# Kernel tuning notes

Hardware: AMD Instinct MI355X
Metric: run time of the kernel (lower is better)

Reference implementation:

```python
import jax, jax.numpy as jnp
import numpy as np
import math


def _alibi_slopes(n_heads):
    def pow2_slopes(n):
        start = 2.0 ** (-2.0 ** (-(math.log2(n) - 3)))
        return [start * start ** i for i in range(n)]
    if math.log2(n_heads) % 1 == 0:
        return np.array(pow2_slopes(n_heads), dtype=np.float32)
    closest = 2 ** math.floor(math.log2(n_heads))
    base = pow2_slopes(closest)
    extra = pow2_slopes(2 * closest)[0::2][: n_heads - closest]
    return np.array(base + extra, dtype=np.float32)


def setup_inputs() -> dict:
    key = jax.random.key(0)
    ks = jax.random.split(key, 5)
    B, T, D = 2, 2048, 1024
    scale = 1.0 / math.sqrt(D)
    return {
        "x": jax.random.normal(ks[0], (B, T, D), dtype=jnp.float32),
        "Wq": jax.random.normal(ks[1], (D, D), dtype=jnp.float32) * scale,
        "Wk": jax.random.normal(ks[2], (D, D), dtype=jnp.float32) * scale,
        "Wv": jax.random.normal(ks[3], (D, D), dtype=jnp.float32) * scale,
        "Wo": jax.random.normal(ks[4], (D, D), dtype=jnp.float32) * scale,
        "window": 256,
    }


def reference(x, Wq, Wk, Wv, Wo, window):
    B, T, D = x.shape
    H = 16
    d_k = D // H

    def proj(W):
        # torch nn.Linear: y = x @ W.T ; then (B,T,H,dk) -> (B,H,T,dk)
        return (x @ W.T).reshape(B, T, H, d_k).transpose(0, 2, 1, 3)

    Q, K, V = proj(Wq), proj(Wk), proj(Wv)
    scores = jnp.einsum("bhtk,bhsk->bhts", Q, K) / math.sqrt(d_k)

    pos = jnp.arange(T)
    dist = jnp.abs(pos[None, :] - pos[:, None]).astype(jnp.float32)  # (T,T)
    slopes = jnp.asarray(_alibi_slopes(H))  # (H,)
    alibi = -slopes[:, None, None] * dist  # (H,T,T)
    win_mask = jnp.where(dist > window // 2, -jnp.inf, 0.0)  # (T,T)

    scores = scores + alibi[None] + win_mask[None, None]
    attn = jax.nn.softmax(scores, axis=-1)  # dropout=0.0 (eval)
    out = jnp.einsum("bhts,bhsd->bthd", attn, V).reshape(B, T, D)
    return out @ Wo.T, attn
```

## Files before the change

### kernel.cpp

```cpp
#include <hip/hip_runtime.h>
#include <hip/hip_bf16.h>


typedef __bf16 bf16x8 __attribute__((ext_vector_type(8)));
typedef float f32x4 __attribute__((ext_vector_type(4)));

__device__ __forceinline__ float bf2f(unsigned short u) {
    union { unsigned int i; float f; } v; v.i = ((unsigned int)u) << 16; return v.f;
}
__device__ __forceinline__ unsigned short f2bf(float f) {
    union { float f; unsigned int i; } v; v.f = f;
    unsigned int r = v.i + 0x7FFFu + ((v.i >> 16) & 1u);
    return (unsigned short)(r >> 16);
}

__global__ __launch_bounds__(256) void cast_all(
    const float* __restrict__ x,
    const float* __restrict__ wq, const float* __restrict__ wk,
    const float* __restrict__ wv, const float* __restrict__ wo,
    unsigned short* __restrict__ xb, unsigned short* __restrict__ wb)
{
    const int slice = blockIdx.y;
    const int i = (blockIdx.x * 256 + threadIdx.x) * 4;
    const float* src;
    unsigned short* dst;
    if (slice < 4) {
        src = x + (size_t)slice * 1048576;
        dst = xb + (size_t)slice * 1048576;
    } else {
        const float* ws4[4] = {wq, wk, wv, wo};
        src = ws4[slice - 4];
        dst = wb + (size_t)(slice - 4) * 1048576;
    }
    const float4 v = *(const float4*)(src + i);
    ushort4 o;
    o.x = f2bf(v.x); o.y = f2bf(v.y); o.z = f2bf(v.z); o.w = f2bf(v.w);
    *(ushort4*)(dst + i) = o;
}

#define GLDS16(g, l) __builtin_amdgcn_global_load_lds(                      \
    (const __attribute__((address_space(1))) void*)(g),                     \
    (__attribute__((address_space(3))) void*)(l), 16, 0, 0)

__global__ __launch_bounds__(256) void gemm_bf16_nt(
    const unsigned short* __restrict__ A, const unsigned short* __restrict__ Bm,
    float* __restrict__ C, unsigned short* __restrict__ qkv,
    int M, int N, int K, int mode)
{
    __shared__ __align__(16) unsigned short As[128 * 32];
    __shared__ __align__(16) unsigned short Bs[128 * 32];

    const int tid  = threadIdx.x;
    const int lane = tid & 63, w = tid >> 6;
    const int bm = blockIdx.y * 128, bn = blockIdx.x * 128;

    const unsigned short* ga = A  + (size_t)(bm + w * 16 + (lane >> 2)) * K + (lane & 3) * 8;
    const unsigned short* gb = Bm + (size_t)(bn + w * 16 + (lane >> 2)) * K + (lane & 3) * 8;
    unsigned short* laA0 = &As[w * 512];
    unsigned short* laA1 = &As[2048 + w * 512];
    unsigned short* laB0 = &Bs[w * 512];
    unsigned short* laB1 = &Bs[2048 + w * 512];

    const int wr = w >> 1, wc = w & 1;
    const int fr = lane & 15, fq = lane >> 4;

    f32x4 acc[4][4] = {};

    for (int k0 = 0; k0 < K; k0 += 32) {
        GLDS16(ga + k0, laA0);
        GLDS16(ga + k0 + (size_t)64 * K, laA1);
        GLDS16(gb + k0, laB0);
        GLDS16(gb + k0 + (size_t)64 * K, laB1);
        __syncthreads();
        bf16x8 af[4], bfv[4];
#pragma unroll
        for (int i = 0; i < 4; ++i)
            af[i] = *(const bf16x8*)&As[(wr * 64 + i * 16 + fr) * 32 + fq * 8];
#pragma unroll
        for (int j = 0; j < 4; ++j)
            bfv[j] = *(const bf16x8*)&Bs[(wc * 64 + j * 16 + fr) * 32 + fq * 8];
#pragma unroll
        for (int i = 0; i < 4; ++i)
#pragma unroll
            for (int j = 0; j < 4; ++j)
                acc[i][j] = __builtin_amdgcn_mfma_f32_16x16x32_bf16(af[i], bfv[j], acc[i][j], 0, 0, 0);
        __syncthreads();
    }

#pragma unroll
    for (int i = 0; i < 4; ++i) {
#pragma unroll
        for (int j = 0; j < 4; ++j) {
            const int mb = bm + wr * 64 + i * 16 + fq * 4;
            const int n  = bn + wc * 64 + j * 16 + fr;
#pragma unroll
            for (int r = 0; r < 4; ++r) {
                const int m = mb + r;
                const float val = acc[i][j][r];
                if (mode == 0) {
                    C[(size_t)m * N + n] = val;
                } else {
                    const int which = n >> 10, hh = (n >> 6) & 15, dd = n & 63;
                    const int bb = m >> 11, tt = m & 2047;
                    size_t off;
                    if (which == 2)
                        off = (size_t)2 * 4194304 + (((size_t)bb * 16 + hh) * 64 + dd) * 2048 + tt;
                    else
                        off = (size_t)which * 4194304 + (((size_t)bb * 16 + hh) * 2048 + tt) * 64 + dd;
                    qkv[off] = f2bf(val);
                }
            }
        }
    }
}

#define NT_MAX 20
__global__ __launch_bounds__(256) void attn_mfma(
    const unsigned short* __restrict__ Q, const unsigned short* __restrict__ K,
    const unsigned short* __restrict__ VT, float* __restrict__ attn,
    unsigned short* __restrict__ ao, const int* __restrict__ wptr)
{
    const int T = 2048;
    __shared__ __align__(16) unsigned short Plds[4][16][328];

    const int bid = (int)blockIdx.x;
    const int swz = (bid & 7) * 128 + (bid >> 3);
    const int w = threadIdx.x >> 6, lane = threadIdx.x & 63;
    const int fr = lane & 15, fq = lane >> 4;

    const int tblk = swz & 31;
    const int h    = (swz >> 5) & 15;
    const int b    = swz >> 9;
    const int t0   = tblk * 64;

    const int W2 = wptr[0] >> 1;
    const int sA = (t0 - W2) > 0 ? (t0 - W2) : 0;
    int sB = t0 + 63 + W2; if (sB > T - 1) sB = T - 1;
    const int sEnd = sB + 1;
    const int nt  = (sEnd - sA) >> 4;
    const int ncc = (nt + 1) >> 1;

    const size_t bhT = ((size_t)b * 16 + h) * T;
    const unsigned short* Qbh  = Q  + bhT * 64;
    const unsigned short* Kbh  = K  + bhT * 64;
    const unsigned short* VTbh = VT + (((size_t)b * 16 + h) * 64) * T;

    bf16x8 aq0 = *(const bf16x8*)(Qbh + (size_t)(t0 + w * 16 + fr) * 64 + fq * 8);
    bf16x8 aq1 = *(const bf16x8*)(Qbh + (size_t)(t0 + w * 16 + fr) * 64 + 32 + fq * 8);

    const float slope = exp2f(-0.5f * (float)(h + 1));
    const int trow0 = t0 + w * 16 + fq * 4;

    f32x4 sc[NT_MAX];
#pragma unroll
    for (int st = 0; st < NT_MAX; ++st) {
        const int sbase = sA + st * 16;
        if (sbase < sEnd) {
            const unsigned short* kb = Kbh + (size_t)(sbase + fr) * 64 + fq * 8;
            bf16x8 b0 = *(const bf16x8*)(kb);
            bf16x8 b1 = *(const bf16x8*)(kb + 32);
            f32x4 sv = {0.f, 0.f, 0.f, 0.f};
            sv = __builtin_amdgcn_mfma_f32_16x16x32_bf16(aq0, b0, sv, 0, 0, 0);
            sv = __builtin_amdgcn_mfma_f32_16x16x32_bf16(aq1, b1, sv, 0, 0, 0);
            const int scol = sbase + fr;
#pragma unroll
            for (int rr = 0; rr < 4; ++rr) {
                const int d = trow0 + rr - scol;
                const int ad = d < 0 ? -d : d;
                const float val = sv[rr] * 0.125f - slope * (float)ad;
                sc[st][rr] = (ad <= W2) ? val : -1e30f;
            }
        } else {
            sc[st] = (f32x4){-1e30f, -1e30f, -1e30f, -1e30f};
        }
    }

    {
        const float4 z4 = {0.f, 0.f, 0.f, 0.f};
        for (int i = 0; i < 16; ++i) {
            float* row = attn + (bhT + t0 + w * 16 + i) * T;
            for (int c = lane * 4; c < sA; c += 256) *(float4*)(row + c) = z4;
            for (int c = sEnd + lane * 4; c < T; c += 256) *(float4*)(row + c) = z4;
        }
    }

    float inv[4];
#pragma unroll
    for (int rr = 0; rr < 4; ++rr) {
        float m = -1e30f;
#pragma unroll
        for (int st = 0; st < NT_MAX; ++st) m = fmaxf(m, sc[st][rr]);
#pragma unroll
        for (int off = 1; off < 16; off <<= 1) m = fmaxf(m, __shfl_xor(m, off, 64));
        float s = 0.f;
#pragma unroll
        for (int st = 0; st < NT_MAX; ++st) {
            const float p = __expf(sc[st][rr] - m);
            sc[st][rr] = p;
            s += p;
        }
#pragma unroll
        for (int off = 1; off < 16; off <<= 1) s += __shfl_xor(s, off, 64);
        inv[rr] = 1.0f / s;
    }

#pragma unroll
    for (int st = 0; st < NT_MAX; ++st) {
        const int sbase = sA + st * 16;
        if (sbase < sEnd) {
#pragma unroll
            for (int rr = 0; rr < 4; ++rr)
                Plds[w][fq * 4 + rr][st * 16 + fr] = f2bf(sc[st][rr] * inv[rr]);
        } else {
#pragma unroll
            for (int rr = 0; rr < 4; ++rr)
                Plds[w][fq * 4 + rr][st * 16 + fr] = 0;
        }
    }

    for (int i = 0; i < 16; ++i) {
        float* row = attn + (bhT + t0 + w * 16 + i) * T;
        const unsigned short* prow = &Plds[w][i][0];
#pragma unroll
        for (int jj = 0; jj < 2; ++jj) {
            const int pc = (jj * 64 + lane) * 4;
            const int c = sA + pc;
            if (c < sEnd) {
                float4 v;
                v.x = bf2f(prow[pc + 0]);
                v.y = bf2f(prow[pc + 1]);
                v.z = bf2f(prow[pc + 2]);
                v.w = bf2f(prow[pc + 3]);
                *(float4*)(row + c) = v;
            }
        }
    }

    f32x4 oacc[4] = {};
    for (int c = 0; c < ncc; ++c) {
        const bf16x8 pa = *(const bf16x8*)&Plds[w][fr][c * 32 + fq * 8];
#pragma unroll
        for (int j = 0; j < 4; ++j) {
            const bf16x8 bv = *(const bf16x8*)(VTbh + (size_t)(j * 16 + fr) * T + sA + c * 32 + fq * 8);
            oacc[j] = __builtin_amdgcn_mfma_f32_16x16x32_bf16(pa, bv, oacc[j], 0, 0, 0);
        }
    }

#pragma unroll
    for (int j = 0; j < 4; ++j)
#pragma unroll
        for (int rr = 0; rr < 4; ++rr)
            ao[((size_t)b * T + trow0 + rr) * 1024 + h * 64 + j * 16 + fr] = f2bf(oacc[j][rr]);
}

extern "C" void kernel_launch(void* const* d_in, const int* in_sizes, int n_in,
                              void* d_out, int out_size, void* d_ws, size_t ws_size,
                              hipStream_t stream)
{
    const float* x  = (const float*)d_in[0];
    const float* Wq = (const float*)d_in[1];
    const float* Wk = (const float*)d_in[2];
    const float* Wv = (const float*)d_in[3];
    const float* Wo = (const float*)d_in[4];
    const int*  win = (const int*)d_in[5];

    const int M = 4096, D = 1024;

    unsigned short* xb    = (unsigned short*)d_ws;
    unsigned short* Wqkvb = xb + (size_t)M * D;
    unsigned short* Wob   = Wqkvb + (size_t)3 * D * D;
    unsigned short* QKVb  = Wob + (size_t)D * D;
    unsigned short* AOb   = QKVb + (size_t)3 * M * D;

    float* out  = (float*)d_out;
    float* attn = out + (size_t)M * D;

    {
        dim3 g(1024, 8);
        cast_all<<<g, 256, 0, stream>>>(x, Wq, Wk, Wv, Wo, xb, Wqkvb);
    }

    {
        dim3 g(3072 / 128, M / 128);
        gemm_bf16_nt<<<g, 256, 0, stream>>>(xb, Wqkvb, nullptr, QKVb, M, 3072, D, 1);
    }

    attn_mfma<<<1024, 256, 0, stream>>>(
        QKVb, QKVb + (size_t)M * D, QKVb + (size_t)2 * M * D, attn, AOb, win);

    {
        dim3 g(D / 128, M / 128);
        gemm_bf16_nt<<<g, 256, 0, stream>>>(AOb, Wob, out, nullptr, M, D, D, 0);
    }
}
```

Measured before the change: 217.6 us.

## Stage QKV epilogue through LDS and move attn zero-fill into GEMMs

The QKV projection epilogue now writes bf16 results into an LDS tile, transposed for the V slice, and then emits 16-byte vectorized stores instead of scattered 2-byte stores. The zero-fill of the out-of-window region of the attention matrix moves out of the attention kernel and is split across the two GEMM launches, each block zeroing 64 rows. This spreads the large write traffic over GEMM blocks that have spare bandwidth. In exchange it adds about 34 KB of LDS per GEMM block, which can lower occupancy, and it hard-codes the window bounds (tb-128 to tb+192) in the GEMM.

```diff
diff --git a/kernel.cpp b/kernel.cpp
--- a/kernel.cpp
+++ b/kernel.cpp
@@ -45,10 +45,12 @@
 __global__ __launch_bounds__(256) void gemm_bf16_nt(
     const unsigned short* __restrict__ A, const unsigned short* __restrict__ Bm,
     float* __restrict__ C, unsigned short* __restrict__ qkv,
+    float* __restrict__ zbuf, int zbase,
     int M, int N, int K, int mode)
 {
     __shared__ __align__(16) unsigned short As[128 * 32];
     __shared__ __align__(16) unsigned short Bs[128 * 32];
+    __shared__ __align__(16) unsigned short Cs[128][136];
 
     const int tid  = threadIdx.x;
     const int lane = tid & 63, w = tid >> 6;
@@ -87,30 +89,84 @@
         __syncthreads();
     }
 
-#pragma unroll
-    for (int i = 0; i < 4; ++i) {
-#pragma unroll
-        for (int j = 0; j < 4; ++j) {
-            const int mb = bm + wr * 64 + i * 16 + fq * 4;
-            const int n  = bn + wc * 64 + j * 16 + fr;
-#pragma unroll
-            for (int r = 0; r < 4; ++r) {
-                const int m = mb + r;
-                const float val = acc[i][j][r];
-                if (mode == 0) {
-                    C[(size_t)m * N + n] = val;
-                } else {
-                    const int which = n >> 10, hh = (n >> 6) & 15, dd = n & 63;
-                    const int bb = m >> 11, tt = m & 2047;
-                    size_t off;
-                    if (which == 2)
-                        off = (size_t)2 * 4194304 + (((size_t)bb * 16 + hh) * 64 + dd) * 2048 + tt;
-                    else
-                        off = (size_t)which * 4194304 + (((size_t)bb * 16 + hh) * 2048 + tt) * 64 + dd;
-                    qkv[off] = f2bf(val);
+    if (mode == 1) {
+        const int which = bn >> 10;
+#pragma unroll
+        for (int i = 0; i < 4; ++i)
+#pragma unroll
+            for (int j = 0; j < 4; ++j) {
+                const int lr = wr * 64 + i * 16 + fq * 4;
+                const int lc = wc * 64 + j * 16 + fr;
+#pragma unroll
+                for (int r = 0; r < 4; ++r) {
+                    const unsigned short bv = f2bf(acc[i][j][r]);
+                    if (which == 2) Cs[lc][lr + r] = bv;
+                    else            Cs[lr + r][lc] = bv;
                 }
             }
-        }
+        __syncthreads();
+
+        {
+            const int lin = (int)(blockIdx.y * gridDim.x + blockIdx.x);
+            const int zrow0 = zbase + lin * 64;
+            const float4 z4 = {0.f, 0.f, 0.f, 0.f};
+            for (int i = 0; i < 16; ++i) {
+                const int row = zrow0 + w * 16 + i;
+                const int tb = (row & 2047) & ~63;
+                int bs = tb - 128; if (bs < 0) bs = 0;
+                const int be = (tb + 192 > 2048) ? 2048 : (tb + 192);
+                float* rp = zbuf + (size_t)row * 2048;
+                for (int c = lane * 4; c < bs; c += 256) *(float4*)(rp + c) = z4;
+                for (int c = be + lane * 4; c < 2048; c += 256) *(float4*)(rp + c) = z4;
+            }
+        }
+
+#pragma unroll
+        for (int rep = 0; rep < 8; ++rep) {
+            const int c2 = rep * 256 + tid;
+            const int row = c2 >> 4, cc = (c2 & 15) * 8;
+            const bf16x8 vv = *(const bf16x8*)&Cs[row][cc];
+            if (which == 2) {
+                const int n = bn + row;
+                const int hh = (n >> 6) & 15, dd = n & 63;
+                const int mm = bm + cc;
+                const int bb = mm >> 11, tt = mm & 2047;
+                *(bf16x8*)(qkv + (size_t)2 * 4194304 +
+                           (((size_t)bb * 16 + hh) * 64 + dd) * 2048 + tt) = vv;
+            } else {
+                const int n = bn + cc;
+                const int hh = (n >> 6) & 15, dd = n & 63;
+                const int mm = bm + row;
+                const int bb = mm >> 11, tt = mm & 2047;
+                *(bf16x8*)(qkv + (size_t)which * 4194304 +
+                           (((size_t)bb * 16 + hh) * 2048 + tt) * 64 + dd) = vv;
+            }
+        }
+    } else {
+        {
+            const int lin = (int)(blockIdx.y * gridDim.x + blockIdx.x);
+            const int zrow0 = zbase + lin * 64;
+            const float4 z4 = {0.f, 0.f, 0.f, 0.f};
+            for (int i = 0; i < 16; ++i) {
+                const int row = zrow0 + w * 16 + i;
+                const int tb = (row & 2047) & ~63;
+                int bs = tb - 128; if (bs < 0) bs = 0;
+                const int be = (tb + 192 > 2048) ? 2048 : (tb + 192);
+                float* rp = zbuf + (size_t)row * 2048;
+                for (int c = lane * 4; c < bs; c += 256) *(float4*)(rp + c) = z4;
+                for (int c = be + lane * 4; c < 2048; c += 256) *(float4*)(rp + c) = z4;
+            }
+        }
+#pragma unroll
+        for (int i = 0; i < 4; ++i)
+#pragma unroll
+            for (int j = 0; j < 4; ++j) {
+                const int mb = bm + wr * 64 + i * 16 + fq * 4;
+                const int n  = bn + wc * 64 + j * 16 + fr;
+#pragma unroll
+                for (int r = 0; r < 4; ++r)
+                    C[(size_t)(mb + r) * N + n] = acc[i][j][r];
+            }
     }
 }
 
@@ -175,15 +231,6 @@
         }
     }
 
-    {
-        const float4 z4 = {0.f, 0.f, 0.f, 0.f};
-        for (int i = 0; i < 16; ++i) {
-            float* row = attn + (bhT + t0 + w * 16 + i) * T;
-            for (int c = lane * 4; c < sA; c += 256) *(float4*)(row + c) = z4;
-            for (int c = sEnd + lane * 4; c < T; c += 256) *(float4*)(row + c) = z4;
-        }
-    }
-
     float inv[4];
 #pragma unroll
     for (int rr = 0; rr < 4; ++rr) {
@@ -282,7 +329,8 @@
 
     {
         dim3 g(3072 / 128, M / 128);
-        gemm_bf16_nt<<<g, 256, 0, stream>>>(xb, Wqkvb, nullptr, QKVb, M, 3072, D, 1);
+        gemm_bf16_nt<<<g, 256, 0, stream>>>(xb, Wqkvb, nullptr, QKVb,
+                                            attn, 0, M, 3072, D, 1);
     }
 
     attn_mfma<<<1024, 256, 0, stream>>>(
@@ -290,6 +338,7 @@
 
     {
         dim3 g(D / 128, M / 128);
-        gemm_bf16_nt<<<g, 256, 0, stream>>>(AOb, Wob, out, nullptr, M, D, D, 0);
-    }
-}
+        gemm_bf16_nt<<<g, 256, 0, stream>>>(AOb, Wob, out, nullptr,
+                                            attn, 49152, M, D, D, 0);
+    }
+}
```

Result: slower. 237.7 us (+9.3%).

## Split attention zero-fill between QKV GEMM epilogue and attention kernel

Applied to the files above, without the earlier changes.

Half of the out-of-window zero writes to the attention-probability matrix move from the attention kernel into the tail of the QKV projection GEMM. The first 512 GEMM blocks each fill the first 32 rows of two 64-row query tiles, and the attention kernel now fills only the remaining 32 rows of its own tile. The goal is to overlap these large bandwidth-bound stores with GEMM compute and shorten the attention kernel. Total bytes written stay the same, and the extra work on a subset of GEMM blocks can unbalance that launch.

```diff
diff --git a/kernel.cpp b/kernel.cpp
--- a/kernel.cpp
+++ b/kernel.cpp
@@ -45,6 +45,7 @@
 __global__ __launch_bounds__(256) void gemm_bf16_nt(
     const unsigned short* __restrict__ A, const unsigned short* __restrict__ Bm,
     float* __restrict__ C, unsigned short* __restrict__ qkv,
+    float* __restrict__ zfill, const int* __restrict__ wptr,
     int M, int N, int K, int mode)
 {
     __shared__ __align__(16) unsigned short As[128 * 32];
@@ -85,6 +86,26 @@
             for (int j = 0; j < 4; ++j)
                 acc[i][j] = __builtin_amdgcn_mfma_f32_16x16x32_bf16(af[i], bfv[j], acc[i][j], 0, 0, 0);
         __syncthreads();
+    }
+
+    if (mode == 1) {
+        const int lin = (int)(blockIdx.y * gridDim.x + blockIdx.x);
+        if (lin < 512) {
+            const int W2f = wptr[0] >> 1;
+            const float4 z4 = {0.f, 0.f, 0.f, 0.f};
+#pragma unroll
+            for (int uu = 0; uu < 2; ++uu) {
+                const int u = 2 * lin + uu;
+                const int t0f = (u << 6) & 2047;
+                const int sAf = (t0f - W2f) > 0 ? (t0f - W2f) : 0;
+                int sEf = t0f + 64 + W2f; if (sEf > 2048) sEf = 2048;
+                for (int k = 0; k < 8; ++k) {
+                    float* rp = zfill + (size_t)(u * 64 + w * 8 + k) * 2048;
+                    for (int c = lane * 4; c < sAf; c += 256) *(float4*)(rp + c) = z4;
+                    for (int c = sEf + lane * 4; c < 2048; c += 256) *(float4*)(rp + c) = z4;
+                }
+            }
+        }
     }
 
 #pragma unroll
@@ -177,10 +198,10 @@
 
     {
         const float4 z4 = {0.f, 0.f, 0.f, 0.f};
-        for (int i = 0; i < 16; ++i) {
-            float* row = attn + (bhT + t0 + w * 16 + i) * T;
-            for (int c = lane * 4; c < sA; c += 256) *(float4*)(row + c) = z4;
-            for (int c = sEnd + lane * 4; c < T; c += 256) *(float4*)(row + c) = z4;
+        for (int k = 0; k < 8; ++k) {
+            float* rp = attn + (bhT + t0 + 32 + w * 8 + k) * T;
+            for (int c = lane * 4; c < sA; c += 256) *(float4*)(rp + c) = z4;
+            for (int c = sEnd + lane * 4; c < T; c += 256) *(float4*)(rp + c) = z4;
         }
     }
 
@@ -282,7 +303,8 @@
 
     {
         dim3 g(3072 / 128, M / 128);
-        gemm_bf16_nt<<<g, 256, 0, stream>>>(xb, Wqkvb, nullptr, QKVb, M, 3072, D, 1);
+        gemm_bf16_nt<<<g, 256, 0, stream>>>(xb, Wqkvb, nullptr, QKVb,
+                                            attn, win, M, 3072, D, 1);
     }
 
     attn_mfma<<<1024, 256, 0, stream>>>(
@@ -290,6 +312,7 @@
 
     {
         dim3 g(D / 128, M / 128);
-        gemm_bf16_nt<<<g, 256, 0, stream>>>(AOb, Wob, out, nullptr, M, D, D, 0);
-    }
-}
+        gemm_bf16_nt<<<g, 256, 0, stream>>>(AOb, Wob, out, nullptr,
+                                            nullptr, win, M, D, D, 0);
+    }
+}
```

Result: slower. 239.4 us (+10.0%).

## Move attention-matrix zero fill into cast and QKV GEMM kernels

Applied to the files above, without the earlier changes.

The attention kernel no longer zeroes the out-of-window parts of the attn rows. Instead, the cast kernel and the QKV projection GEMM now together write zeros over the entire attn buffer, split into fixed per-block chunks. The attention kernel later overwrites the in-band region. The aim is to hide the large zero-store traffic behind the GEMM's compute instead of serialising it in the attention kernel. In exchange, the in-band region is now written twice, the chunk offsets are hard-coded to these sizes, and the GEMM's inner loop gains global stores that may compete with its own loads.

```diff
diff --git a/kernel.cpp b/kernel.cpp
--- a/kernel.cpp
+++ b/kernel.cpp
@@ -18,10 +18,12 @@
     const float* __restrict__ x,
     const float* __restrict__ wq, const float* __restrict__ wk,
     const float* __restrict__ wv, const float* __restrict__ wo,
-    unsigned short* __restrict__ xb, unsigned short* __restrict__ wb)
+    unsigned short* __restrict__ xb, unsigned short* __restrict__ wb,
+    float4* __restrict__ zf)
 {
     const int slice = blockIdx.y;
-    const int i = (blockIdx.x * 256 + threadIdx.x) * 4;
+    const int tid = threadIdx.x;
+    const int i = (blockIdx.x * 256 + tid) * 4;
     const float* src;
     unsigned short* dst;
     if (slice < 4) {
@@ -36,6 +38,12 @@
     ushort4 o;
     o.x = f2bf(v.x); o.y = f2bf(v.y); o.z = f2bf(v.z); o.w = f2bf(v.w);
     *(ushort4*)(dst + i) = o;
+
+    const int bflat = slice * 1024 + blockIdx.x;
+    float4* zp = zf + (size_t)bflat * 1792 + tid;
+    const float4 z4 = {0.f, 0.f, 0.f, 0.f};
+#pragma unroll
+    for (int k = 0; k < 7; ++k) zp[k * 256] = z4;
 }
 
 #define GLDS16(g, l) __builtin_amdgcn_global_load_lds(                      \
@@ -45,6 +53,7 @@
 __global__ __launch_bounds__(256) void gemm_bf16_nt(
     const unsigned short* __restrict__ A, const unsigned short* __restrict__ Bm,
     float* __restrict__ C, unsigned short* __restrict__ qkv,
+    float4* __restrict__ zf,
     int M, int N, int K, int mode)
 {
     __shared__ __align__(16) unsigned short As[128 * 32];
@@ -64,6 +73,12 @@
     const int wr = w >> 1, wc = w & 1;
     const int fr = lane & 15, fq = lane >> 4;
 
+    float4* zp0 = nullptr;
+    if (zf) {
+        const int lin = (int)(blockIdx.y * gridDim.x + blockIdx.x);
+        zp0 = zf + (size_t)lin * 24576 + tid;
+    }
+
     f32x4 acc[4][4] = {};
 
     for (int k0 = 0; k0 < K; k0 += 32) {
@@ -72,6 +87,13 @@
         GLDS16(gb + k0, laB0);
         GLDS16(gb + k0 + (size_t)64 * K, laB1);
         __syncthreads();
+
+        if (zp0) {
+            const float4 z4 = {0.f, 0.f, 0.f, 0.f};
+            float4* zp = zp0 + (size_t)(k0 >> 5) * 768;
+            zp[0] = z4; zp[256] = z4; zp[512] = z4;
+        }
+
         bf16x8 af[4], bfv[4];
 #pragma unroll
         for (int i = 0; i < 4; ++i)
@@ -175,15 +197,6 @@
         }
     }
 
-    {
-        const float4 z4 = {0.f, 0.f, 0.f, 0.f};
-        for (int i = 0; i < 16; ++i) {
-            float* row = attn + (bhT + t0 + w * 16 + i) * T;
-            for (int c = lane * 4; c < sA; c += 256) *(float4*)(row + c) = z4;
-            for (int c = sEnd + lane * 4; c < T; c += 256) *(float4*)(row + c) = z4;
-        }
-    }
-
     float inv[4];
 #pragma unroll
     for (int rr = 0; rr < 4; ++rr) {
@@ -275,14 +288,18 @@
     float* out  = (float*)d_out;
     float* attn = out + (size_t)M * D;
 
+    float4* zf_cast = (float4*)attn;
+    float4* zf_gemm = (float4*)attn + 14680064;
+
     {
         dim3 g(1024, 8);
-        cast_all<<<g, 256, 0, stream>>>(x, Wq, Wk, Wv, Wo, xb, Wqkvb);
+        cast_all<<<g, 256, 0, stream>>>(x, Wq, Wk, Wv, Wo, xb, Wqkvb, zf_cast);
     }
 
     {
         dim3 g(3072 / 128, M / 128);
-        gemm_bf16_nt<<<g, 256, 0, stream>>>(xb, Wqkvb, nullptr, QKVb, M, 3072, D, 1);
+        gemm_bf16_nt<<<g, 256, 0, stream>>>(xb, Wqkvb, nullptr, QKVb,
+                                            zf_gemm, M, 3072, D, 1);
     }
 
     attn_mfma<<<1024, 256, 0, stream>>>(
@@ -290,6 +307,7 @@
 
     {
         dim3 g(D / 128, M / 128);
-        gemm_bf16_nt<<<g, 256, 0, stream>>>(AOb, Wob, out, nullptr, M, D, D, 0);
-    }
-}
+        gemm_bf16_nt<<<g, 256, 0, stream>>>(AOb, Wob, out, nullptr,
+                                            nullptr, M, D, D, 0);
+    }
+}
```

Result: slower. 240.0 us (+10.3%).
